# Kernel tuning notes

Measured on AMD Instinct MI355X. Metric: run time of the kernel, lower is better.

Reference implementation:

```python
import jax, jax.numpy as jnp
import numpy as np

# Static configuration (matches init_kwargs)
NW, WH, WW, SH, SW = 1024, 8, 8, 2, 2
EMBED, NH = 192, 6
HD = EMBED // NH            # 32
NP = WH * WW                # 64 patches per window
S2 = SH * SW                # 4 shuffle groups
L = NP * S2                 # 256 tokens per window
NWM = 64                    # number of mask windows
SCALE = HD ** (-0.5) / SH   # head_dim**-0.5 / shuffle
EPS = 1e-5


def _rel_pos_index():
    # Swin-style relative position index for an (8,8) window.
    coords = np.stack(np.meshgrid(np.arange(WH), np.arange(WW), indexing='ij')).reshape(2, -1)
    rel = (coords[:, :, None] - coords[:, None, :]).transpose(1, 2, 0)  # (64,64,2)
    rel[..., 0] += WH - 1
    rel[..., 0] *= 2 * WW - 1
    rel[..., 1] += WW - 1
    return jnp.asarray(rel.sum(-1).reshape(-1))  # (4096,) values in [0, 225)

REL_IDX = _rel_pos_index()


def _group(x):
    # 'nw (wh sh ww sw) ch -> nw (wh ww) (sh sw) ch'
    return x.reshape(NW, WH, SH, WW, SW, EMBED).transpose(0, 1, 3, 2, 4, 5).reshape(NW, NP, S2, EMBED)


def _ungroup(x):
    # 'nw (wh ww) (sh sw) ch -> nw (wh sh ww sw) ch'
    return x.reshape(NW, WH, WW, SH, SW, EMBED).transpose(0, 1, 3, 2, 4, 5).reshape(NW, L, EMBED)


def _ln(x, w, b):
    # LayerNorm over the last two dims [shuffle**2, embed_dim]
    mu = x.mean(axis=(-2, -1), keepdims=True)
    var = x.var(axis=(-2, -1), keepdims=True)
    return (x - mu) * jax.lax.rsqrt(var + EPS) * w + b


def _heads(x):
    # 'nw np s2 (nh hd) -> nw nh np s2 hd'
    return x.reshape(NW, NP, S2, NH, HD).transpose(0, 3, 1, 2, 4)


def setup_inputs() -> dict:
    key = jax.random.key(0)
    ks = jax.random.split(key, 7)
    inp = {
        'query': jax.random.normal(ks[0], (NW, L, EMBED), jnp.float32),
        'key': jax.random.normal(ks[1], (NW, L, EMBED), jnp.float32),
        'value': jax.random.normal(ks[2], (NW, L, EMBED), jnp.float32),
        'mask': jax.random.normal(ks[3], (NWM, NP, NP), jnp.float32),
        'ln_q_w': jnp.ones((S2, EMBED), jnp.float32),
        'ln_q_b': jnp.zeros((S2, EMBED), jnp.float32),
        'ln_k_w': jnp.ones((S2, EMBED), jnp.float32),
        'ln_k_b': jnp.zeros((S2, EMBED), jnp.float32),
        'ln_v_w': jnp.ones((S2, EMBED), jnp.float32),
        'ln_v_b': jnp.zeros((S2, EMBED), jnp.float32),
        'bias_table': 0.02 * jax.random.normal(ks[4], ((2 * WH - 1) * (2 * WW - 1), NH), jnp.float32),
        'proj_w': 0.02 * jax.random.normal(ks[5], (EMBED, EMBED), jnp.float32),  # nn.Linear weight (out,in)
    }
    return inp


def reference(query, key, value, mask, ln_q_w, ln_q_b, ln_k_w, ln_k_b, ln_v_w, ln_v_b, bias_table, proj_w):
    q = _heads(_ln(_group(query), ln_q_w, ln_q_b)) * SCALE   # (nw,nh,np,s2,hd)
    k = _heads(_ln(_group(key), ln_k_w, ln_k_b))
    v = _heads(_ln(_group(value), ln_v_w, ln_v_b))

    attn = jnp.einsum('whqsc,whksc->whqk', q, k)              # (nw,nh,np,np)

    bias = bias_table[REL_IDX].reshape(NP, NP, NH).transpose(2, 0, 1)  # (nh,np,np)
    attn = attn + bias[None]

    b = NW // NWM
    attn = (attn.reshape(b, NWM, NH, NP, NP) + mask[None, :, None]).reshape(NW, NH, NP, NP)

    attn = jax.nn.softmax(attn, axis=-1)

    out = jnp.einsum('whqk,whksc->whqsc', attn, v)            # (nw,nh,np,s2,hd)
    out = out.transpose(0, 2, 3, 1, 4).reshape(NW, NP, S2, EMBED)
    out = _ungroup(out)                                       # (nw, L, embed)
    return out @ proj_w.T
```

## Files before the change

### kernel.cpp

```cpp
#include <hip/hip_runtime.h>

#define NWIN 1024
#define LTOK 256
#define EMB  192
#define NPAT 64
#define NHEAD 6
#define HDIM 32
#define SCALE 0.08838834764831845f
#define LN_EPS 1e-5f

typedef float f32x4 __attribute__((ext_vector_type(4)));
typedef short s16x8 __attribute__((ext_vector_type(8)));

#define OFF_PRE 0
#define OFF_KH  98304
#define OFF_VT  114688
#define OFF_PB  131072
#define OFF_SB  139264
#define OFF_ST  156672
#define OFF_BH  158208
#define SMEM_BYTES 159168
#define OFF_WL  OFF_KH

__device__ __forceinline__ unsigned short f2bf(float f) {
    unsigned u = __float_as_uint(f);
    u += 0x7fffu + ((u >> 16) & 1u);
    return (unsigned short)(u >> 16);
}

__device__ __forceinline__ int tok_of(int p, int s) {
    return ((p >> 3) << 5) + ((s >> 1) << 4) + ((p & 7) << 1) + (s & 1);
}

__device__ __forceinline__ f32x4 mfma16(s16x8 a, s16x8 b, f32x4 c) {
    return __builtin_amdgcn_mfma_f32_16x16x32_bf16(a, b, c, 0, 0, 0);
}

__device__ __forceinline__ s16x8 ln_pack8(const float* __restrict__ x,
                                          float mu, float rs,
                                          const float* __restrict__ wl,
                                          const float* __restrict__ bl,
                                          float scale) {
    f32x4 a  = *(const f32x4*)x;
    f32x4 b  = *(const f32x4*)(x + 4);
    f32x4 w0 = *(const f32x4*)wl;
    f32x4 w1 = *(const f32x4*)(wl + 4);
    f32x4 c0 = *(const f32x4*)bl;
    f32x4 c1 = *(const f32x4*)(bl + 4);
    s16x8 r;
    r[0] = (short)f2bf(((a[0]-mu)*rs*w0[0] + c0[0])*scale);
    r[1] = (short)f2bf(((a[1]-mu)*rs*w0[1] + c0[1])*scale);
    r[2] = (short)f2bf(((a[2]-mu)*rs*w0[2] + c0[2])*scale);
    r[3] = (short)f2bf(((a[3]-mu)*rs*w0[3] + c0[3])*scale);
    r[4] = (short)f2bf(((b[0]-mu)*rs*w1[0] + c1[0])*scale);
    r[5] = (short)f2bf(((b[1]-mu)*rs*w1[1] + c1[1])*scale);
    r[6] = (short)f2bf(((b[2]-mu)*rs*w1[2] + c1[2])*scale);
    r[7] = (short)f2bf(((b[3]-mu)*rs*w1[3] + c1[3])*scale);
    return r;
}

__device__ __forceinline__ void ln_f8(const float* __restrict__ x,
                                      float mu, float rs,
                                      const float* __restrict__ wl,
                                      const float* __restrict__ bl,
                                      float* o) {
    f32x4 a  = *(const f32x4*)x;
    f32x4 b  = *(const f32x4*)(x + 4);
    f32x4 w0 = *(const f32x4*)wl;
    f32x4 w1 = *(const f32x4*)(wl + 4);
    f32x4 c0 = *(const f32x4*)bl;
    f32x4 c1 = *(const f32x4*)(bl + 4);
    o[0] = (a[0]-mu)*rs*w0[0] + c0[0];
    o[1] = (a[1]-mu)*rs*w0[1] + c0[1];
    o[2] = (a[2]-mu)*rs*w0[2] + c0[2];
    o[3] = (a[3]-mu)*rs*w0[3] + c0[3];
    o[4] = (b[0]-mu)*rs*w1[0] + c1[0];
    o[5] = (b[1]-mu)*rs*w1[1] + c1[1];
    o[6] = (b[2]-mu)*rs*w1[2] + c1[2];
    o[7] = (b[3]-mu)*rs*w1[3] + c1[3];
}

__global__ __launch_bounds__(512, 2) void dwa_kernel(
    const float* __restrict__ q_g, const float* __restrict__ k_g,
    const float* __restrict__ v_g, const float* __restrict__ mask_g,
    const float* __restrict__ lnqw, const float* __restrict__ lnqb,
    const float* __restrict__ lnkw, const float* __restrict__ lnkb,
    const float* __restrict__ lnvw, const float* __restrict__ lnvb,
    const float* __restrict__ btab, const float* __restrict__ pw,
    float* __restrict__ out_g)
{
    __shared__ __align__(16) char smem[SMEM_BYTES];

    const int tid  = threadIdx.x;
    const int lane = tid & 63;
    const int wv   = tid >> 6;
    const int win  = blockIdx.x;
    const size_t wbase = (size_t)win * LTOK * EMB;

    float* stats = (float*)(smem + OFF_ST);
    float* muq = stats;       float* rsq = stats + 64;
    float* muk = stats + 128; float* rsk = stats + 192;
    float* muv = stats + 256; float* rsv = stats + 320;
    float* biash = (float*)(smem + OFF_BH);

    {
        const float* tens[3] = {q_g, k_g, v_g};
        float* part = (float*)(smem + OFF_SB);
        const int t = tid >> 1, half = tid & 1;
        for (int x = 0; x < 3; ++x) {
            const f32x4* ptr = (const f32x4*)(tens[x] + wbase + t * EMB + half * 96);
            float s1 = 0.f, s2 = 0.f;
            #pragma unroll
            for (int i = 0; i < 24; ++i) {
                f32x4 v = ptr[i];
                s1 += v[0] + v[1] + v[2] + v[3];
                s2 += v[0]*v[0] + v[1]*v[1] + v[2]*v[2] + v[3]*v[3];
            }
            part[(t*2 + half)*2 + 0] = s1;
            part[(t*2 + half)*2 + 1] = s2;
            __syncthreads();
            if (tid < NPAT) {
                float S1 = 0.f, S2 = 0.f;
                #pragma unroll
                for (int s = 0; s < 4; ++s) {
                    int tt = tok_of(tid, s);
                    S1 += part[tt*4 + 0] + part[tt*4 + 2];
                    S2 += part[tt*4 + 1] + part[tt*4 + 3];
                }
                float mu  = S1 * (1.f/768.f);
                float var = S2 * (1.f/768.f) - mu*mu;
                stats[x*128 + tid]      = mu;
                stats[x*128 + 64 + tid] = rsqrtf(var + LN_EPS);
            }
            __syncthreads();
        }
    }

    const int mwin = win & 63;
    const float* mask_w = mask_g + (size_t)mwin * NPAT * NPAT;

    for (int h = 0; h < NHEAD; ++h) {
        __syncthreads();

        if (tid < 225) biash[tid] = btab[tid * NHEAD + h];

        #pragma unroll
        for (int i = 0; i < 2; ++i) {
            int c   = tid * 2 + i;
            int p   = c >> 4;
            int scb = c & 15;
            int s   = scb >> 2;
            int co  = (scb & 3) * 8;
            int t   = tok_of(p, s);
            int chb = h * HDIM + co;

            {
                const float* kp = k_g + wbase + t*EMB + chb;
                s16x8 kk = ln_pack8(kp, muk[p], rsk[p],
                                    lnkw + s*EMB + chb, lnkb + s*EMB + chb, 1.0f);
                *(s16x8*)(smem + OFF_KH + p*256 + ((scb*16) ^ ((p & 7) << 4))) = kk;
            }
            {
                const float* vp = v_g + wbase + t*EMB + chb;
                float vn[8];
                ln_f8(vp, muv[p], rsv[p], lnvw + s*EMB + chb, lnvb + s*EMB + chb, vn);
                #pragma unroll
                for (int j = 0; j < 8; ++j) {
                    int sc = scb*8 + j;
                    *(unsigned short*)(smem + OFF_VT + sc*128 + ((p*2) ^ ((sc & 7) << 4)))
                        = f2bf(vn[j]);
                }
            }
        }
        __syncthreads();

        {
            int mstrip = wv >> 1, nhalf = wv & 1;
            int pr = mstrip*16 + (lane & 15);
            int cb = lane >> 4;
            float mu = muq[pr], rs = rsq[pr];
            f32x4 acc0 = {0.f,0.f,0.f,0.f};
            f32x4 acc1 = {0.f,0.f,0.f,0.f};
            #pragma unroll
            for (int ks = 0; ks < 4; ++ks) {
                int s = ks;
                int t = tok_of(pr, s);
                int chb = h*HDIM + cb*8;
                s16x8 af = ln_pack8(q_g + wbase + t*EMB + chb, mu, rs,
                                    lnqw + s*EMB + chb, lnqb + s*EMB + chb, SCALE);
                {
                    int row = (nhalf*2 + 0)*16 + (lane & 15);
                    s16x8 bf = *(const s16x8*)(smem + OFF_KH + row*256 +
                                  ((ks*64 + cb*16) ^ ((row & 7) << 4)));
                    acc0 = mfma16(af, bf, acc0);
                }
                {
                    int row = (nhalf*2 + 1)*16 + (lane & 15);
                    s16x8 bf = *(const s16x8*)(smem + OFF_KH + row*256 +
                                  ((ks*64 + cb*16) ^ ((row & 7) << 4)));
                    acc1 = mfma16(af, bf, acc1);
                }
            }
            float* Sb = (float*)(smem + OFF_SB);
            #pragma unroll
            for (int r = 0; r < 4; ++r) {
                int qr = mstrip*16 + (lane >> 4)*4 + r;
                Sb[qr*68 + (nhalf*2+0)*16 + (lane & 15)] = acc0[r];
                Sb[qr*68 + (nhalf*2+1)*16 + (lane & 15)] = acc1[r];
            }
        }
        __syncthreads();

        {
            int qr = tid >> 3, j = tid & 7;
            const float* Sb = (const float*)(smem + OFF_SB);
            f32x4 s0 = *(const f32x4*)(Sb + qr*68 + j*8);
            f32x4 s1 = *(const f32x4*)(Sb + qr*68 + j*8 + 4);
            f32x4 m0 = *(const f32x4*)(mask_w + qr*64 + j*8);
            f32x4 m1 = *(const f32x4*)(mask_w + qr*64 + j*8 + 4);
            int qh = qr >> 3, qw = qr & 7;
            float vals[8];
            #pragma unroll
            for (int jj = 0; jj < 8; ++jj) {
                int kc = j*8 + jj;
                int idx = (qh - (kc >> 3) + 7)*15 + (qw - (kc & 7) + 7);
                float sv = (jj < 4 ? s0[jj] : s1[jj-4]) +
                           (jj < 4 ? m0[jj] : m1[jj-4]) + biash[idx];
                vals[jj] = sv;
            }
            float mx = vals[0];
            #pragma unroll
            for (int jj = 1; jj < 8; ++jj) mx = fmaxf(mx, vals[jj]);
            mx = fmaxf(mx, __shfl_xor(mx, 1));
            mx = fmaxf(mx, __shfl_xor(mx, 2));
            mx = fmaxf(mx, __shfl_xor(mx, 4));
            float sum = 0.f;
            #pragma unroll
            for (int jj = 0; jj < 8; ++jj) { vals[jj] = __expf(vals[jj] - mx); sum += vals[jj]; }
            sum += __shfl_xor(sum, 1);
            sum += __shfl_xor(sum, 2);
            sum += __shfl_xor(sum, 4);
            float rinv = 1.f / sum;
            s16x8 pv;
            #pragma unroll
            for (int jj = 0; jj < 8; ++jj) pv[jj] = (short)f2bf(vals[jj] * rinv);
            *(s16x8*)(smem + OFF_PB + qr*128 + ((j*16) ^ ((qr & 7) << 4))) = pv;
        }
        __syncthreads();

        {
            int m = wv >> 1, nset = wv & 1;
            int cb = lane >> 4;
            int prow = m*16 + (lane & 15);
            s16x8 ap0 = *(const s16x8*)(smem + OFF_PB + prow*128 +
                          ((0*64 + cb*16) ^ ((prow & 7) << 4)));
            s16x8 ap1 = *(const s16x8*)(smem + OFF_PB + prow*128 +
                          ((1*64 + cb*16) ^ ((prow & 7) << 4)));
            #pragma unroll
            for (int i = 0; i < 4; ++i) {
                int nt = nset*4 + i;
                int brow = nt*16 + (lane & 15);
                f32x4 acc = {0.f,0.f,0.f,0.f};
                s16x8 bf0 = *(const s16x8*)(smem + OFF_VT + brow*128 +
                              ((0*64 + cb*16) ^ ((brow & 7) << 4)));
                s16x8 bf1 = *(const s16x8*)(smem + OFF_VT + brow*128 +
                              ((1*64 + cb*16) ^ ((brow & 7) << 4)));
                acc = mfma16(ap0, bf0, acc);
                acc = mfma16(ap1, bf1, acc);
                int sc = nt*16 + (lane & 15);
                int s  = sc >> 5, c2 = sc & 31;
                int ch = h*HDIM + c2;
                #pragma unroll
                for (int r = 0; r < 4; ++r) {
                    int qp = m*16 + (lane >> 4)*4 + r;
                    int t  = tok_of(qp, s);
                    *(unsigned short*)(smem + OFF_PRE + t*384 + ((ch*2) ^ ((t & 7) << 4)))
                        = f2bf(acc[r]);
                }
            }
        }
    }

    for (int np = 0; np < 2; ++np) {
        __syncthreads();
        for (int c = tid; c < 96*24; c += 512) {
            int o = c / 24, cb8 = c % 24;
            const float* wp = pw + (size_t)(np*96 + o)*EMB + cb8*8;
            f32x4 a = *(const f32x4*)wp;
            f32x4 b = *(const f32x4*)(wp + 4);
            s16x8 w8;
            w8[0] = (short)f2bf(a[0]); w8[1] = (short)f2bf(a[1]);
            w8[2] = (short)f2bf(a[2]); w8[3] = (short)f2bf(a[3]);
            w8[4] = (short)f2bf(b[0]); w8[5] = (short)f2bf(b[1]);
            w8[6] = (short)f2bf(b[2]); w8[7] = (short)f2bf(b[3]);
            *(s16x8*)(smem + OFF_WL + o*384 + ((cb8*16) ^ ((o & 7) << 4))) = w8;
        }
        __syncthreads();

        int cb = lane >> 4;
        #pragma unroll
        for (int mi = 0; mi < 2; ++mi) {
            int mt = wv*2 + mi;
            int arow = mt*16 + (lane & 15);
            s16x8 af[6];
            #pragma unroll
            for (int ks = 0; ks < 6; ++ks) {
                af[ks] = *(const s16x8*)(smem + OFF_PRE + arow*384 +
                              ((ks*64 + cb*16) ^ ((arow & 7) << 4)));
            }
            #pragma unroll
            for (int nt = 0; nt < 6; ++nt) {
                int orow = nt*16 + (lane & 15);
                f32x4 acc = {0.f,0.f,0.f,0.f};
                #pragma unroll
                for (int ks = 0; ks < 6; ++ks) {
                    s16x8 bf = *(const s16x8*)(smem + OFF_WL + orow*384 +
                                  ((ks*64 + cb*16) ^ ((orow & 7) << 4)));
                    acc = mfma16(af[ks], bf, acc);
                }
                int oc = np*96 + nt*16 + (lane & 15);
                #pragma unroll
                for (int r = 0; r < 4; ++r) {
                    int trow = mt*16 + (lane >> 4)*4 + r;
                    out_g[wbase + trow*EMB + oc] = acc[r];
                }
            }
        }
    }
}

extern "C" void kernel_launch(void* const* d_in, const int* in_sizes, int n_in,
                              void* d_out, int out_size, void* d_ws, size_t ws_size,
                              hipStream_t stream) {
    (void)in_sizes; (void)n_in; (void)out_size; (void)d_ws; (void)ws_size;
    dwa_kernel<<<dim3(NWIN), dim3(512), 0, stream>>>(
        (const float*)d_in[0],  (const float*)d_in[1],  (const float*)d_in[2],
        (const float*)d_in[3],  (const float*)d_in[4],  (const float*)d_in[5],
        (const float*)d_in[6],  (const float*)d_in[7],  (const float*)d_in[8],
        (const float*)d_in[9],  (const float*)d_in[10], (const float*)d_in[11],
        (float*)d_out);
}
```

Measured before the change: 386.5 us.

## Split projection into separate kernel, stage pre-projection activations in output buffer

The fused kernel is split in two. The attention kernel no longer holds the full 96KB pre-projection tile in LDS. Instead it writes bf16 per-head results into the upper half of each output row in global memory, which shrinks LDS to about 60KB and raises launch bounds to 4 blocks per CU. A second kernel reads that staging area, converts proj weights to bf16 on the fly, and writes the fp32 outputs in place. The LN statistics pass is also merged into one loop over q, k and v, and the K/V load mapping is reordered. The cost is an extra global round trip, a second launch, and reliance on in-place aliasing where each 16-row strip's reads must finish before its writes overlap.

```diff
diff --git a/kernel.cpp b/kernel.cpp
--- a/kernel.cpp
+++ b/kernel.cpp
@@ -12,15 +12,13 @@
 typedef float f32x4 __attribute__((ext_vector_type(4)));
 typedef short s16x8 __attribute__((ext_vector_type(8)));
 
-#define OFF_PRE 0
-#define OFF_KH  98304
-#define OFF_VT  114688
-#define OFF_PB  131072
-#define OFF_SB  139264
-#define OFF_ST  156672
-#define OFF_BH  158208
-#define SMEM_BYTES 159168
-#define OFF_WL  OFF_KH
+#define OFF_KH  0
+#define OFF_VT  16384
+#define OFF_PB  32768
+#define OFF_SB  40960
+#define OFF_ST  58368
+#define OFF_BH  59904
+#define SMEM_BYTES 60928
 
 __device__ __forceinline__ unsigned short f2bf(float f) {
     unsigned u = __float_as_uint(f);
@@ -80,14 +78,14 @@
     o[7] = (b[3]-mu)*rs*w1[3] + c1[3];
 }
 
-__global__ __launch_bounds__(512, 2) void dwa_kernel(
+
+__global__ __launch_bounds__(512, 4) void dwa_attn_kernel(
     const float* __restrict__ q_g, const float* __restrict__ k_g,
     const float* __restrict__ v_g, const float* __restrict__ mask_g,
     const float* __restrict__ lnqw, const float* __restrict__ lnqb,
     const float* __restrict__ lnkw, const float* __restrict__ lnkb,
     const float* __restrict__ lnvw, const float* __restrict__ lnvb,
-    const float* __restrict__ btab, const float* __restrict__ pw,
-    float* __restrict__ out_g)
+    const float* __restrict__ btab, float* __restrict__ out_g)
 {
     __shared__ __align__(16) char smem[SMEM_BYTES];
 
@@ -96,6 +94,7 @@
     const int wv   = tid >> 6;
     const int win  = blockIdx.x;
     const size_t wbase = (size_t)win * LTOK * EMB;
+    char* preb = (char*)out_g + (size_t)win * 196608;
 
     float* stats = (float*)(smem + OFF_ST);
     float* muq = stats;       float* rsq = stats + 64;
@@ -104,71 +103,77 @@
     float* biash = (float*)(smem + OFF_BH);
 
     {
-        const float* tens[3] = {q_g, k_g, v_g};
         float* part = (float*)(smem + OFF_SB);
         const int t = tid >> 1, half = tid & 1;
-        for (int x = 0; x < 3; ++x) {
-            const f32x4* ptr = (const f32x4*)(tens[x] + wbase + t * EMB + half * 96);
-            float s1 = 0.f, s2 = 0.f;
-            #pragma unroll
-            for (int i = 0; i < 24; ++i) {
-                f32x4 v = ptr[i];
-                s1 += v[0] + v[1] + v[2] + v[3];
-                s2 += v[0]*v[0] + v[1]*v[1] + v[2]*v[2] + v[3]*v[3];
-            }
-            part[(t*2 + half)*2 + 0] = s1;
-            part[(t*2 + half)*2 + 1] = s2;
-            __syncthreads();
-            if (tid < NPAT) {
-                float S1 = 0.f, S2 = 0.f;
+        const f32x4* qp = (const f32x4*)(q_g + wbase + t*EMB + half*96);
+        const f32x4* kp = (const f32x4*)(k_g + wbase + t*EMB + half*96);
+        const f32x4* vp = (const f32x4*)(v_g + wbase + t*EMB + half*96);
+        float s1q=0.f,s2q=0.f,s1k=0.f,s2k=0.f,s1v=0.f,s2v=0.f;
+        #pragma unroll 4
+        for (int i = 0; i < 24; ++i) {
+            f32x4 a = qp[i];
+            s1q += a[0]+a[1]+a[2]+a[3];
+            s2q += a[0]*a[0]+a[1]*a[1]+a[2]*a[2]+a[3]*a[3];
+            f32x4 b = kp[i];
+            s1k += b[0]+b[1]+b[2]+b[3];
+            s2k += b[0]*b[0]+b[1]*b[1]+b[2]*b[2]+b[3]*b[3];
+            f32x4 c = vp[i];
+            s1v += c[0]+c[1]+c[2]+c[3];
+            s2v += c[0]*c[0]+c[1]*c[1]+c[2]*c[2]+c[3]*c[3];
+        }
+        float* pp = part + (t*2 + half)*6;
+        pp[0]=s1q; pp[1]=s2q; pp[2]=s1k; pp[3]=s2k; pp[4]=s1v; pp[5]=s2v;
+        __syncthreads();
+        if (tid < NPAT) {
+            float S[6] = {0.f,0.f,0.f,0.f,0.f,0.f};
+            #pragma unroll
+            for (int s = 0; s < 4; ++s) {
+                int tt = tok_of(tid, s);
+                const float* pr = part + tt*12;
                 #pragma unroll
-                for (int s = 0; s < 4; ++s) {
-                    int tt = tok_of(tid, s);
-                    S1 += part[tt*4 + 0] + part[tt*4 + 2];
-                    S2 += part[tt*4 + 1] + part[tt*4 + 3];
-                }
-                float mu  = S1 * (1.f/768.f);
-                float var = S2 * (1.f/768.f) - mu*mu;
+                for (int x = 0; x < 6; ++x) S[x] += pr[x] + pr[6 + x];
+            }
+            #pragma unroll
+            for (int x = 0; x < 3; ++x) {
+                float mu  = S[2*x] * (1.f/768.f);
+                float var = S[2*x+1] * (1.f/768.f) - mu*mu;
                 stats[x*128 + tid]      = mu;
                 stats[x*128 + 64 + tid] = rsqrtf(var + LN_EPS);
             }
-            __syncthreads();
-        }
+        }
+        __syncthreads();
     }
 
     const int mwin = win & 63;
     const float* mask_w = mask_g + (size_t)mwin * NPAT * NPAT;
 
     for (int h = 0; h < NHEAD; ++h) {
-        __syncthreads();
-
         if (tid < 225) biash[tid] = btab[tid * NHEAD + h];
-
-        #pragma unroll
-        for (int i = 0; i < 2; ++i) {
-            int c   = tid * 2 + i;
-            int p   = c >> 4;
-            int scb = c & 15;
-            int s   = scb >> 2;
-            int co  = (scb & 3) * 8;
-            int t   = tok_of(p, s);
-            int chb = h * HDIM + co;
-
-            {
-                const float* kp = k_g + wbase + t*EMB + chb;
-                s16x8 kk = ln_pack8(kp, muk[p], rsk[p],
-                                    lnkw + s*EMB + chb, lnkb + s*EMB + chb, 1.0f);
-                *(s16x8*)(smem + OFF_KH + p*256 + ((scb*16) ^ ((p & 7) << 4))) = kk;
-            }
-            {
-                const float* vp = v_g + wbase + t*EMB + chb;
-                float vn[8];
-                ln_f8(vp, muv[p], rsv[p], lnvw + s*EMB + chb, lnvb + s*EMB + chb, vn);
-                #pragma unroll
-                for (int j = 0; j < 8; ++j) {
-                    int sc = scb*8 + j;
-                    *(unsigned short*)(smem + OFF_VT + sc*128 + ((p*2) ^ ((sc & 7) << 4)))
-                        = f2bf(vn[j]);
+        {
+            const int p = tid & 63;
+            #pragma unroll
+            for (int i = 0; i < 2; ++i) {
+                int scb = (tid >> 6) * 2 + i;
+                int s   = scb >> 2;
+                int co  = (scb & 3) * 8;
+                int t   = tok_of(p, s);
+                int chb = h * HDIM + co;
+                {
+                    const float* kp = k_g + wbase + t*EMB + chb;
+                    s16x8 kk = ln_pack8(kp, muk[p], rsk[p],
+                                        lnkw + s*EMB + chb, lnkb + s*EMB + chb, 1.0f);
+                    *(s16x8*)(smem + OFF_KH + p*256 + ((scb*16) ^ ((p & 7) << 4))) = kk;
+                }
+                {
+                    const float* vp = v_g + wbase + t*EMB + chb;
+                    float vn[8];
+                    ln_f8(vp, muv[p], rsv[p], lnvw + s*EMB + chb, lnvb + s*EMB + chb, vn);
+                    #pragma unroll
+                    for (int j = 0; j < 8; ++j) {
+                        int sc = scb*8 + j;
+                        *(unsigned short*)(smem + OFF_VT + sc*128 + ((p*2) ^ ((sc & 7) << 4)))
+                            = f2bf(vn[j]);
+                    }
                 }
             }
         }
@@ -268,63 +273,70 @@
                 acc = mfma16(ap0, bf0, acc);
                 acc = mfma16(ap1, bf1, acc);
                 int sc = nt*16 + (lane & 15);
-                int s  = sc >> 5, c2 = sc & 31;
-                int ch = h*HDIM + c2;
                 #pragma unroll
                 for (int r = 0; r < 4; ++r) {
                     int qp = m*16 + (lane >> 4)*4 + r;
-                    int t  = tok_of(qp, s);
-                    *(unsigned short*)(smem + OFF_PRE + t*384 + ((ch*2) ^ ((t & 7) << 4)))
+                    *(unsigned short*)(smem + OFF_SB + qp*256 + ((sc*2) ^ ((qp & 7) << 4)))
                         = f2bf(acc[r]);
                 }
             }
         }
+        __syncthreads();
+
+        #pragma unroll
+        for (int i = 0; i < 2; ++i) {
+            int c   = tid*2 + i;
+            int qp  = c >> 4;
+            int s   = (c >> 2) & 3;
+            int c2b = c & 3;
+            s16x8 v = *(const s16x8*)(smem + OFF_SB + qp*256 +
+                          (((s*64 + c2b*16)) ^ ((qp & 7) << 4)));
+            int t = tok_of(qp, s);
+            *(s16x8*)(preb + (size_t)t*768 + 384 + h*64 + c2b*16) = v;
+        }
     }
-
-    for (int np = 0; np < 2; ++np) {
-        __syncthreads();
-        for (int c = tid; c < 96*24; c += 512) {
-            int o = c / 24, cb8 = c % 24;
-            const float* wp = pw + (size_t)(np*96 + o)*EMB + cb8*8;
-            f32x4 a = *(const f32x4*)wp;
-            f32x4 b = *(const f32x4*)(wp + 4);
-            s16x8 w8;
-            w8[0] = (short)f2bf(a[0]); w8[1] = (short)f2bf(a[1]);
-            w8[2] = (short)f2bf(a[2]); w8[3] = (short)f2bf(a[3]);
-            w8[4] = (short)f2bf(b[0]); w8[5] = (short)f2bf(b[1]);
-            w8[6] = (short)f2bf(b[2]); w8[7] = (short)f2bf(b[3]);
-            *(s16x8*)(smem + OFF_WL + o*384 + ((cb8*16) ^ ((o & 7) << 4))) = w8;
-        }
-        __syncthreads();
-
-        int cb = lane >> 4;
+}
+
+__global__ __launch_bounds__(256, 4) void dwa_proj_kernel(
+    const float* __restrict__ pw, float* __restrict__ out_g)
+{
+    const int tid  = threadIdx.x;
+    const int lane = tid & 63;
+    const int wv   = tid >> 6;
+    const int g    = blockIdx.x * 4 + wv;
+    const int w    = g >> 4;
+    const int strip = g & 15;
+    const char* preb = (const char*)out_g + (size_t)w * 196608;
+
+    const int cb = lane >> 4;
+    const int arow = strip*16 + (lane & 15);
+
+    s16x8 af[6];
+    #pragma unroll
+    for (int ks = 0; ks < 6; ++ks) {
+        af[ks] = *(const s16x8*)(preb + (size_t)arow*768 + 384 + ks*64 + cb*16);
+    }
+
+    #pragma unroll
+    for (int nt = 0; nt < 12; ++nt) {
+        int orow = nt*16 + (lane & 15);
+        const float* wp = pw + (size_t)orow*EMB + cb*8;
+        f32x4 acc = {0.f,0.f,0.f,0.f};
         #pragma unroll
-        for (int mi = 0; mi < 2; ++mi) {
-            int mt = wv*2 + mi;
-            int arow = mt*16 + (lane & 15);
-            s16x8 af[6];
-            #pragma unroll
-            for (int ks = 0; ks < 6; ++ks) {
-                af[ks] = *(const s16x8*)(smem + OFF_PRE + arow*384 +
-                              ((ks*64 + cb*16) ^ ((arow & 7) << 4)));
-            }
-            #pragma unroll
-            for (int nt = 0; nt < 6; ++nt) {
-                int orow = nt*16 + (lane & 15);
-                f32x4 acc = {0.f,0.f,0.f,0.f};
-                #pragma unroll
-                for (int ks = 0; ks < 6; ++ks) {
-                    s16x8 bf = *(const s16x8*)(smem + OFF_WL + orow*384 +
-                                  ((ks*64 + cb*16) ^ ((orow & 7) << 4)));
-                    acc = mfma16(af[ks], bf, acc);
-                }
-                int oc = np*96 + nt*16 + (lane & 15);
-                #pragma unroll
-                for (int r = 0; r < 4; ++r) {
-                    int trow = mt*16 + (lane >> 4)*4 + r;
-                    out_g[wbase + trow*EMB + oc] = acc[r];
-                }
-            }
+        for (int ks = 0; ks < 6; ++ks) {
+            f32x4 a = *(const f32x4*)(wp + ks*32);
+            f32x4 b = *(const f32x4*)(wp + ks*32 + 4);
+            s16x8 bf;
+            bf[0] = (short)f2bf(a[0]); bf[1] = (short)f2bf(a[1]);
+            bf[2] = (short)f2bf(a[2]); bf[3] = (short)f2bf(a[3]);
+            bf[4] = (short)f2bf(b[0]); bf[5] = (short)f2bf(b[1]);
+            bf[6] = (short)f2bf(b[2]); bf[7] = (short)f2bf(b[3]);
+            acc = mfma16(af[ks], bf, acc);
+        }
+        #pragma unroll
+        for (int r = 0; r < 4; ++r) {
+            int trow = strip*16 + (lane >> 4)*4 + r;
+            out_g[(size_t)w*49152 + trow*EMB + nt*16 + (lane & 15)] = acc[r];
         }
     }
 }
@@ -333,10 +345,12 @@
                               void* d_out, int out_size, void* d_ws, size_t ws_size,
                               hipStream_t stream) {
     (void)in_sizes; (void)n_in; (void)out_size; (void)d_ws; (void)ws_size;
-    dwa_kernel<<<dim3(NWIN), dim3(512), 0, stream>>>(
+    dwa_attn_kernel<<<dim3(NWIN), dim3(512), 0, stream>>>(
         (const float*)d_in[0],  (const float*)d_in[1],  (const float*)d_in[2],
         (const float*)d_in[3],  (const float*)d_in[4],  (const float*)d_in[5],
         (const float*)d_in[6],  (const float*)d_in[7],  (const float*)d_in[8],
-        (const float*)d_in[9],  (const float*)d_in[10], (const float*)d_in[11],
+        (const float*)d_in[9],  (const float*)d_in[10],
         (float*)d_out);
-}
+    dwa_proj_kernel<<<dim3(NWIN*4), dim3(256), 0, stream>>>(
+        (const float*)d_in[11], (float*)d_out);
+}
```

Result: slower. 690.5 us (+78.7%).
